# Performance work log

Measured on AMD Instinct MI355X. Metric: run time of the kernel, lower is better.

Reference implementation:

```python
import jax, jax.numpy as jnp
import numpy as np

N = 50000
E = 800000
C = 128   # embed_channels
H = 4     # num_heads
D = C // H
POS = 3


def setup_inputs() -> dict:
    key = jax.random.key(0)
    ks = jax.random.split(key, 8)
    feat = jax.random.normal(ks[0], (N, C), dtype=jnp.float32)
    coord = jax.random.normal(ks[1], (N, POS), dtype=jnp.float32)
    graph = jax.random.randint(ks[2], (2, E), 0, N, dtype=jnp.int32)
    qkv_w = jax.random.normal(ks[3], (3 * C, C), dtype=jnp.float32) * (1.0 / np.sqrt(C))
    qkv_b = jax.random.normal(ks[4], (3 * C,), dtype=jnp.float32) * 0.02
    rpe_w = jax.random.normal(ks[5], (C, POS), dtype=jnp.float32) * (1.0 / np.sqrt(POS))
    rpe_b = jax.random.normal(ks[6], (C,), dtype=jnp.float32) * 0.02
    return {"feat": feat, "coord": coord, "graph": graph,
            "qkv_w": qkv_w, "qkv_b": qkv_b, "rpe_w": rpe_w, "rpe_b": rpe_b}


def _segment_softmax(x, seg, n):
    # x: [E, H], seg: [E] -> softmax over edges sharing the same destination node
    seg_max = jax.ops.segment_max(x, seg, num_segments=n)          # [N, H]
    seg_max = jnp.where(jnp.isfinite(seg_max), seg_max, 0.0)
    ex = jnp.exp(x - seg_max[seg])                                 # [E, H]
    seg_sum = jax.ops.segment_sum(ex, seg, num_segments=n)         # [N, H]
    return ex / seg_sum[seg]


def reference(feat, coord, graph, qkv_w, qkv_b, rpe_w, rpe_b):
    n = feat.shape[0]
    # qkv projection: [N, 3C] -> [N, 3, H, D]
    qkv = (feat @ qkv_w.T + qkv_b).reshape(n, 3, H, D)
    query, key, value = qkv[:, 0], qkv[:, 1], qkv[:, 2]            # each [N, H, D]
    dst, src = graph[0], graph[1]                                  # [E]
    # relative position encoding per edge
    rel = coord[dst] - coord[src]                                  # [E, 3]
    rpe = (rel @ rpe_w.T + rpe_b).reshape(-1, H, D)                # [E, H, D]
    # per-edge attention logits
    attn = (key[src] * query[dst] + rpe).sum(-1)                   # [E, H]
    attn = _segment_softmax(attn, dst, n)                          # [E, H]
    # weighted scatter-sum of values
    msg = attn[..., None] * value[src]                             # [E, H, D]
    out = jax.ops.segment_sum(msg, dst, num_segments=n)            # [N, H, D]
    return out.reshape(n, H * D)
```

## Files before the change

kernel.cpp:

```cpp
#include <hip/hip_runtime.h>
#include <hip/hip_bf16.h>

#define NN 50000
#define NE 800000
#define PAD 64
#define CAB 196

typedef _Float16 fp16x8 __attribute__((ext_vector_type(8)));
typedef _Float16 half2 __attribute__((ext_vector_type(2)));
typedef __attribute__((ext_vector_type(8))) unsigned short ushort8;
typedef __attribute__((ext_vector_type(4))) float f32x4;

static __device__ __forceinline__ unsigned short f2h(float x) {
    _Float16 h = (_Float16)x;
    return __builtin_bit_cast(unsigned short, h);
}
static __device__ __forceinline__ float dot2(half2 a, half2 b, float c) {
#if __has_builtin(__builtin_amdgcn_fdot2)
    return __builtin_amdgcn_fdot2(a, b, c, false);
#else
    return c + (float)a.x * (float)b.x + (float)a.y * (float)b.y;
#endif
}

__global__ __launch_bounds__(256) void qkv_gemm(
    const float* __restrict__ feat, const float* __restrict__ w,
    const float* __restrict__ bias, unsigned short* __restrict__ qbuf16,
    unsigned short* __restrict__ kvbuf,
    const float* __restrict__ coord, const float* __restrict__ rpe_w,
    const float* __restrict__ rpe_b, float* __restrict__ ca,
    float* __restrict__ cb,
    const int* __restrict__ graph, int* __restrict__ cnt,
    unsigned short* __restrict__ sorted_src)
{
    const int t    = threadIdx.x;
    const int role = blockIdx.x & 3;
    const int bi   = blockIdx.x >> 2;

    if (role == 3) {
        if (bi < CAB) {
            __shared__ float s_rw[12];
            __shared__ float s_rb[4];
            if (t < 12) {
                int h = t / 3, p = t % 3;
                float s = 0.f;
                for (int d = 0; d < 32; ++d) s += rpe_w[(h * 32 + d) * 3 + p];
                s_rw[t] = s;
            } else if (t < 16) {
                int h = t - 12;
                float s = 0.f;
                for (int d = 0; d < 32; ++d) s += rpe_b[h * 32 + d];
                s_rb[h] = s;
            }
            __syncthreads();
            int n = bi * 256 + t;
            if (n < NN) {
                float c0 = coord[n * 3 + 0], c1 = coord[n * 3 + 1], c2 = coord[n * 3 + 2];
#pragma unroll
                for (int h = 0; h < 4; ++h) {
                    float a = c0 * s_rw[h * 3 + 0] + c1 * s_rw[h * 3 + 1] + c2 * s_rw[h * 3 + 2];
                    ca[n * 4 + h] = a;
                    cb[n * 4 + h] = a + s_rb[h];
                }
            }
        }
        const int e0 = bi * 256 + t;
        const int stride = 391 * 256;
        int dsts[8], srcs[8], slots[8];
        bool ok[8];
#pragma unroll
        for (int u = 0; u < 8; ++u) {
            int e = e0 + u * stride;
            ok[u] = (e < NE);
            if (ok[u]) { dsts[u] = graph[e]; srcs[u] = graph[NE + e]; }
        }
#pragma unroll
        for (int u = 0; u < 8; ++u)
            if (ok[u]) slots[u] = atomicAdd(&cnt[dsts[u]], 1);
#pragma unroll
        for (int u = 0; u < 8; ++u)
            if (ok[u] && slots[u] < PAD)
                sorted_src[(dsts[u] << 6) + slots[u]] = (unsigned short)srcs[u];
        return;
    }

    __shared__ __align__(16) unsigned short Ah[128][40];
    __shared__ __align__(16) unsigned short Bh[128][40];

    const int bm = bi * 128;
    const int bc = role * 128;

    const int wave = t >> 6;
    const int lane = t & 63;
    const int wr = wave & 1;
    const int wc = wave >> 1;
    const int qd = lane >> 4;
    const int l15 = lane & 15;

    f32x4 acc[4][4];
#pragma unroll
    for (int i = 0; i < 4; ++i)
#pragma unroll
        for (int j = 0; j < 4; ++j)
            acc[i][j] = (f32x4){0.f, 0.f, 0.f, 0.f};

    for (int ks = 0; ks < 4; ++ks) {
        const int k0 = ks * 32;
        if (ks) __syncthreads();
#pragma unroll
        for (int c = 0; c < 2; ++c) {
            int idx = c * 256 + t;
            int r  = idx >> 2;
            int c8 = (idx & 3) * 8;
            int ga = bm + r;
            ushort8 a8 = (ushort8){0,0,0,0,0,0,0,0};
            if (ga < NN) {
                const float* ap = feat + (size_t)ga * 128 + k0 + c8;
                float4 x = *(const float4*)ap;
                float4 y = *(const float4*)(ap + 4);
                a8 = (ushort8){f2h(x.x), f2h(x.y), f2h(x.z), f2h(x.w),
                               f2h(y.x), f2h(y.y), f2h(y.z), f2h(y.w)};
            }
            *(ushort8*)&Ah[r][c8] = a8;
            const float* bp = w + (size_t)(bc + r) * 128 + k0 + c8;
            float4 bx = *(const float4*)bp;
            float4 by = *(const float4*)(bp + 4);
            *(ushort8*)&Bh[r][c8] = (ushort8){f2h(bx.x), f2h(bx.y), f2h(bx.z), f2h(bx.w),
                                              f2h(by.x), f2h(by.y), f2h(by.z), f2h(by.w)};
        }
        __syncthreads();
        fp16x8 af[4];
#pragma unroll
        for (int i = 0; i < 4; ++i)
            af[i] = *(const fp16x8*)&Ah[wr * 64 + 16 * i + l15][qd * 8];
#pragma unroll
        for (int j = 0; j < 4; ++j) {
            fp16x8 bf = *(const fp16x8*)&Bh[wc * 64 + 16 * j + l15][qd * 8];
#pragma unroll
            for (int i = 0; i < 4; ++i)
                acc[i][j] = __builtin_amdgcn_mfma_f32_16x16x32_f16(af[i], bf, acc[i][j], 0, 0, 0);
        }
    }

    float bj[4];
#pragma unroll
    for (int j = 0; j < 4; ++j)
        bj[j] = bias[bc + wc * 64 + 16 * j + l15];

    unsigned short* Ct = &Ah[0][0];
    const int isQ = (role == 0);
    const int half = (role == 1) ? 0 : 128;
    const int relRowW = wr * 16 + qd * 4;

    for (int i = 0; i < 4; ++i) {
        __syncthreads();
#pragma unroll
        for (int j = 0; j < 4; ++j) {
            int col = wc * 64 + 16 * j + l15;
#pragma unroll
            for (int rg = 0; rg < 4; ++rg)
                Ct[(relRowW + rg) * 136 + col] = f2h(acc[i][j][rg] + bj[j]);
        }
        __syncthreads();
#pragma unroll
        for (int p = 0; p < 2; ++p) {
            int linear = p * 256 + t;
            int rr = linear >> 4;
            int cc = linear & 15;
            int absRow = bm + 16 * i + rr + ((rr >> 4) * 48);
            if (absRow < NN) {
                ushort8 val = *(const ushort8*)&Ct[rr * 136 + cc * 8];
                if (isQ) *(ushort8*)(qbuf16 + (size_t)absRow * 128 + cc * 8) = val;
                else     *(ushort8*)(kvbuf + (size_t)absRow * 256 + half + cc * 8) = val;
            }
        }
    }
}

__global__ __launch_bounds__(256) void node_attn(
    const unsigned short* __restrict__ qbuf16, const unsigned short* __restrict__ kvbuf,
    const float* __restrict__ ca, const float* __restrict__ cb,
    const int* __restrict__ cnt, const unsigned short* __restrict__ sorted_src,
    float* __restrict__ out)
{
    const int t = threadIdx.x;
    const int n = blockIdx.x * 8 + (t >> 5);
    if (n >= NN) return;
    const int j = t & 31;
    const int h = j >> 3;
    const int j8 = j * 8;
    const int h4 = h * 4;

    const uint2 qv = *(const uint2*)((const char*)qbuf16 + (size_t)n * 256 + j8);
    const half2 qh01 = __builtin_bit_cast(half2, qv.x);
    const half2 qh23 = __builtin_bit_cast(half2, qv.y);
    const float cbh = cb[n * 4 + h];
    const int start = n << 6;
    int d = cnt[n];
    if (d > PAD) d = PAD;

    float4 acc = make_float4(0.f, 0.f, 0.f, 0.f);
    float den = 0.f;
    const char* kvp = (const char*)kvbuf;
    const char* cap = (const char*)ca;

    int i = 0;
    for (; i + 3 < d; i += 4) {
        ushort4 s4 = *(const ushort4*)(sorted_src + start + i);
        unsigned o0 = (unsigned)s4.x << 9;
        unsigned o1 = (unsigned)s4.y << 9;
        unsigned o2 = (unsigned)s4.z << 9;
        unsigned o3 = (unsigned)s4.w << 9;
        uint2 k0 = *(const uint2*)(kvp + o0 + j8);
        uint2 k1 = *(const uint2*)(kvp + o1 + j8);
        uint2 k2 = *(const uint2*)(kvp + o2 + j8);
        uint2 k3 = *(const uint2*)(kvp + o3 + j8);
        uint2 v0 = *(const uint2*)(kvp + o0 + 256 + j8);
        uint2 v1 = *(const uint2*)(kvp + o1 + 256 + j8);
        uint2 v2 = *(const uint2*)(kvp + o2 + 256 + j8);
        uint2 v3 = *(const uint2*)(kvp + o3 + 256 + j8);
        float a0 = *(const float*)(cap + (o0 >> 5) + h4);
        float a1 = *(const float*)(cap + (o1 >> 5) + h4);
        float a2 = *(const float*)(cap + (o2 >> 5) + h4);
        float a3 = *(const float*)(cap + (o3 >> 5) + h4);

        float p0 = dot2(qh01, __builtin_bit_cast(half2, k0.x),
                   dot2(qh23, __builtin_bit_cast(half2, k0.y), 0.f));
        float p1 = dot2(qh01, __builtin_bit_cast(half2, k1.x),
                   dot2(qh23, __builtin_bit_cast(half2, k1.y), 0.f));
        float p2 = dot2(qh01, __builtin_bit_cast(half2, k2.x),
                   dot2(qh23, __builtin_bit_cast(half2, k2.y), 0.f));
        float p3 = dot2(qh01, __builtin_bit_cast(half2, k3.x),
                   dot2(qh23, __builtin_bit_cast(half2, k3.y), 0.f));
        p0 += __shfl_xor(p0, 1); p1 += __shfl_xor(p1, 1);
        p2 += __shfl_xor(p2, 1); p3 += __shfl_xor(p3, 1);
        p0 += __shfl_xor(p0, 2); p1 += __shfl_xor(p1, 2);
        p2 += __shfl_xor(p2, 2); p3 += __shfl_xor(p3, 2);
        p0 += __shfl_xor(p0, 4); p1 += __shfl_xor(p1, 4);
        p2 += __shfl_xor(p2, 4); p3 += __shfl_xor(p3, 4);

        float e0 = __expf(p0 + cbh - a0);
        float e1 = __expf(p1 + cbh - a1);
        float e2 = __expf(p2 + cbh - a2);
        float e3 = __expf(p3 + cbh - a3);
        den += (e0 + e1) + (e2 + e3);
        half2 v0a = __builtin_bit_cast(half2, v0.x), v0b = __builtin_bit_cast(half2, v0.y);
        half2 v1a = __builtin_bit_cast(half2, v1.x), v1b = __builtin_bit_cast(half2, v1.y);
        half2 v2a = __builtin_bit_cast(half2, v2.x), v2b = __builtin_bit_cast(half2, v2.y);
        half2 v3a = __builtin_bit_cast(half2, v3.x), v3b = __builtin_bit_cast(half2, v3.y);
        acc.x += e0 * (float)v0a.x + e1 * (float)v1a.x + e2 * (float)v2a.x + e3 * (float)v3a.x;
        acc.y += e0 * (float)v0a.y + e1 * (float)v1a.y + e2 * (float)v2a.y + e3 * (float)v3a.y;
        acc.z += e0 * (float)v0b.x + e1 * (float)v1b.x + e2 * (float)v2b.x + e3 * (float)v3b.x;
        acc.w += e0 * (float)v0b.y + e1 * (float)v1b.y + e2 * (float)v2b.y + e3 * (float)v3b.y;
    }
    for (; i < d; ++i) {
        unsigned o0 = (unsigned)sorted_src[start + i] << 9;
        uint2 k0 = *(const uint2*)(kvp + o0 + j8);
        uint2 v0 = *(const uint2*)(kvp + o0 + 256 + j8);
        float a0 = *(const float*)(cap + (o0 >> 5) + h4);
        float p0 = dot2(qh01, __builtin_bit_cast(half2, k0.x),
                   dot2(qh23, __builtin_bit_cast(half2, k0.y), 0.f));
        p0 += __shfl_xor(p0, 1);
        p0 += __shfl_xor(p0, 2);
        p0 += __shfl_xor(p0, 4);
        float e = __expf(p0 + cbh - a0);
        den += e;
        half2 va = __builtin_bit_cast(half2, v0.x);
        half2 vb = __builtin_bit_cast(half2, v0.y);
        acc.x += e * (float)va.x;
        acc.y += e * (float)va.y;
        acc.z += e * (float)vb.x;
        acc.w += e * (float)vb.y;
    }

    float inv = (den > 0.f) ? 1.0f / den : 0.f;
    float4 o = make_float4(acc.x * inv, acc.y * inv, acc.z * inv, acc.w * inv);
    ((float4*)(out + (size_t)n * 128))[j] = o;
}

extern "C" void kernel_launch(void* const* d_in, const int* in_sizes, int n_in,
                              void* d_out, int out_size, void* d_ws, size_t ws_size,
                              hipStream_t stream) {
    const float* feat  = (const float*)d_in[0];
    const float* coord = (const float*)d_in[1];
    const int*   graph = (const int*)d_in[2];
    const float* qkv_w = (const float*)d_in[3];
    const float* qkv_b = (const float*)d_in[4];
    const float* rpe_w = (const float*)d_in[5];
    const float* rpe_b = (const float*)d_in[6];
    float* out = (float*)d_out;

    unsigned short* qbuf16 = (unsigned short*)d_ws;
    unsigned short* kvbuf  = qbuf16 + (size_t)NN * 128;
    int*            cnt    = (int*)(kvbuf + (size_t)NN * 256);
    unsigned short* sorted_src = (unsigned short*)(cnt + NN);
    float* ca = (float*)(sorted_src + (size_t)NN * PAD);
    float* cb = ca + (size_t)NN * 4;

    hipMemsetAsync(cnt, 0, NN * sizeof(int), stream);

    qkv_gemm <<<dim3(391 * 4), 256, 0, stream>>>(feat, qkv_w, qkv_b, qbuf16, kvbuf,
                                                 coord, rpe_w, rpe_b, ca, cb,
                                                 graph, cnt, sorted_src);
    node_attn<<<dim3((NN + 7) / 8), 256, 0, stream>>>(qbuf16, kvbuf, ca, cb,
                                                      cnt, sorted_src, out);
}
```

Measured before the change: 204.7 us.

## Spread edge bucketing across all blocks, pad counters, unroll gather by eight

Edge bucketing (atomic count plus src placement) moves out of the role-3 blocks only and is spread over every block of the fused GEMM launch, each handling two edges. Per-node counters are padded to a 128-byte stride so that atomics on neighbouring nodes do not share a cache line. The attention loop gains an 8-way unrolled gather to keep more loads in flight. The costs are a memset 32x larger, atomics now sitting in front of GEMM work, and higher register pressure in the attention kernel.

```diff
diff --git a/kernel.cpp b/kernel.cpp
--- a/kernel.cpp
+++ b/kernel.cpp
@@ -5,6 +5,7 @@
 #define NE 800000
 #define PAD 64
 #define CAB 196
+#define CNT_STRIDE 32
 
 typedef _Float16 fp16x8 __attribute__((ext_vector_type(8)));
 typedef _Float16 half2 __attribute__((ext_vector_type(2)));
@@ -36,6 +37,26 @@
     const int t    = threadIdx.x;
     const int role = blockIdx.x & 3;
     const int bi   = blockIdx.x >> 2;
+
+    {
+        const int e0 = blockIdx.x * 256 + t;
+        const int stride = 391 * 4 * 256;
+        int dsts[2], srcs[2], slots[2];
+        bool ok[2];
+#pragma unroll
+        for (int u = 0; u < 2; ++u) {
+            int e = e0 + u * stride;
+            ok[u] = (e < NE);
+            if (ok[u]) { dsts[u] = graph[e]; srcs[u] = graph[NE + e]; }
+        }
+#pragma unroll
+        for (int u = 0; u < 2; ++u)
+            if (ok[u]) slots[u] = atomicAdd(&cnt[dsts[u] * CNT_STRIDE], 1);
+#pragma unroll
+        for (int u = 0; u < 2; ++u)
+            if (ok[u] && slots[u] < PAD)
+                sorted_src[(dsts[u] << 6) + slots[u]] = (unsigned short)srcs[u];
+    }
 
     if (role == 3) {
         if (bi < CAB) {
@@ -64,23 +85,6 @@
                 }
             }
         }
-        const int e0 = bi * 256 + t;
-        const int stride = 391 * 256;
-        int dsts[8], srcs[8], slots[8];
-        bool ok[8];
-#pragma unroll
-        for (int u = 0; u < 8; ++u) {
-            int e = e0 + u * stride;
-            ok[u] = (e < NE);
-            if (ok[u]) { dsts[u] = graph[e]; srcs[u] = graph[NE + e]; }
-        }
-#pragma unroll
-        for (int u = 0; u < 8; ++u)
-            if (ok[u]) slots[u] = atomicAdd(&cnt[dsts[u]], 1);
-#pragma unroll
-        for (int u = 0; u < 8; ++u)
-            if (ok[u] && slots[u] < PAD)
-                sorted_src[(dsts[u] << 6) + slots[u]] = (unsigned short)srcs[u];
         return;
     }
 
@@ -196,7 +200,7 @@
     const half2 qh23 = __builtin_bit_cast(half2, qv.y);
     const float cbh = cb[n * 4 + h];
     const int start = n << 6;
-    int d = cnt[n];
+    int d = cnt[n * CNT_STRIDE];
     if (d > PAD) d = PAD;
 
     float4 acc = make_float4(0.f, 0.f, 0.f, 0.f);
@@ -205,6 +209,43 @@
     const char* cap = (const char*)ca;
 
     int i = 0;
+    for (; i + 7 < d; i += 8) {
+        ushort8 s8 = *(const ushort8*)(sorted_src + start + i);
+        unsigned o[8];
+#pragma unroll
+        for (int u = 0; u < 8; ++u) o[u] = (unsigned)s8[u] << 9;
+        uint2 kk[8], vv[8];
+        float aa[8];
+#pragma unroll
+        for (int u = 0; u < 8; ++u) kk[u] = *(const uint2*)(kvp + o[u] + j8);
+#pragma unroll
+        for (int u = 0; u < 8; ++u) vv[u] = *(const uint2*)(kvp + o[u] + 256 + j8);
+#pragma unroll
+        for (int u = 0; u < 8; ++u) aa[u] = *(const float*)(cap + (o[u] >> 5) + h4);
+        float p[8];
+#pragma unroll
+        for (int u = 0; u < 8; ++u)
+            p[u] = dot2(qh01, __builtin_bit_cast(half2, kk[u].x),
+                   dot2(qh23, __builtin_bit_cast(half2, kk[u].y), 0.f));
+#pragma unroll
+        for (int u = 0; u < 8; ++u) p[u] += __shfl_xor(p[u], 1);
+#pragma unroll
+        for (int u = 0; u < 8; ++u) p[u] += __shfl_xor(p[u], 2);
+#pragma unroll
+        for (int u = 0; u < 8; ++u) p[u] += __shfl_xor(p[u], 4);
+        float e[8];
+#pragma unroll
+        for (int u = 0; u < 8; ++u) { e[u] = __expf(p[u] + cbh - aa[u]); den += e[u]; }
+#pragma unroll
+        for (int u = 0; u < 8; ++u) {
+            half2 va = __builtin_bit_cast(half2, vv[u].x);
+            half2 vb = __builtin_bit_cast(half2, vv[u].y);
+            acc.x += e[u] * (float)va.x;
+            acc.y += e[u] * (float)va.y;
+            acc.z += e[u] * (float)vb.x;
+            acc.w += e[u] * (float)vb.y;
+        }
+    }
     for (; i + 3 < d; i += 4) {
         ushort4 s4 = *(const ushort4*)(sorted_src + start + i);
         unsigned o0 = (unsigned)s4.x << 9;
@@ -293,11 +334,11 @@
     unsigned short* qbuf16 = (unsigned short*)d_ws;
     unsigned short* kvbuf  = qbuf16 + (size_t)NN * 128;
     int*            cnt    = (int*)(kvbuf + (size_t)NN * 256);
-    unsigned short* sorted_src = (unsigned short*)(cnt + NN);
+    unsigned short* sorted_src = (unsigned short*)(cnt + (size_t)NN * CNT_STRIDE);
     float* ca = (float*)(sorted_src + (size_t)NN * PAD);
     float* cb = ca + (size_t)NN * 4;
 
-    hipMemsetAsync(cnt, 0, NN * sizeof(int), stream);
+    hipMemsetAsync(cnt, 0, (size_t)NN * CNT_STRIDE * sizeof(int), stream);
 
     qkv_gemm <<<dim3(391 * 4), 256, 0, stream>>>(feat, qkv_w, qkv_b, qbuf16, kvbuf,
                                                  coord, rpe_w, rpe_b, ca, cb,
```

Result: slower. 212.6 us (+3.9%).
